# Kernel optimization log

Measured on AMD Instinct MI355X. Metric: run time of the kernel, lower is better.

The kernel has to match this reference:

```python
import jax, jax.numpy as jnp
import numpy as np
import math

B, S, H, NH = 2, 2048, 2048, 16
HD = H // NH            # head_dim = 128
SEQ_LENGTH = 1024       # config.seq_length (logn base)
NEG = -1e9


def _rotate_half(x):
    # x: [..., hd]; split into two halves (j=2 layout) and rotate
    d = x.shape[-1] // 2
    x1, x2 = x[..., :d], x[..., d:]
    return jnp.concatenate([-x2, x1], axis=-1)


def _apply_rope(t, cos, sin):
    # t: [B,S,NH,HD], cos/sin: [1,S,1,rot_dim]; rot_dim == HD here (no pass-through)
    return t * cos + _rotate_half(t) * sin


def setup_inputs() -> dict:
    key = jax.random.key(0)
    k0, k1, k2 = jax.random.split(key, 3)
    hidden_states = jax.random.normal(k0, (B, S, H), jnp.float32)

    # rotary cos/sin: QWen-style, freqs duplicated across both halves
    pos = jnp.arange(S, dtype=jnp.float32)
    inv_freq = 1.0 / (10000.0 ** (jnp.arange(0, HD, 2, dtype=jnp.float32) / HD))  # [HD/2]
    ang = pos[:, None] * inv_freq[None, :]                # [S, HD/2]
    ang = jnp.concatenate([ang, ang], axis=-1)[None, :, None, :]  # [1,S,1,HD]
    cos, sin = jnp.cos(ang), jnp.sin(ang)

    # additive causal mask (registered_causal_mask path is unused in _attn)
    causal = jnp.tril(jnp.ones((S, S), dtype=bool))
    attention_mask = jnp.where(causal, 0.0, NEG)[None, None, :, :].astype(jnp.float32)

    # logn scaling vector for positions 1..S
    i = np.arange(1, S + 1)
    logn_np = np.where(i > SEQ_LENGTH, np.log(i) / np.log(SEQ_LENGTH), 1.0).astype(np.float32)
    logn = jnp.asarray(logn_np)[None, :, None, None]      # [1,S,1,1]

    Wc = jax.random.normal(k1, (H, 3 * H), jnp.float32) * 0.02
    bc = jnp.zeros((3 * H,), jnp.float32)
    Wp = jax.random.normal(k2, (H, H), jnp.float32) * 0.02
    bp = jnp.zeros((H,), jnp.float32)
    return {
        "hidden_states": hidden_states, "cos": cos, "sin": sin,
        "attention_mask": attention_mask, "logn": logn,
        "Wc": Wc, "bc": bc, "Wp": Wp, "bp": bp,
    }


def reference(hidden_states, cos, sin, attention_mask, logn, Wc, bc, Wp, bp):
    # QKV projection
    qkv = hidden_states @ Wc + bc                         # [B,S,3H]
    q, k, v = jnp.split(qkv, 3, axis=-1)
    q = q.reshape(B, S, NH, HD)
    k = k.reshape(B, S, NH, HD)
    v = v.reshape(B, S, NH, HD)

    # rotary embedding on q and k
    q = _apply_rope(q, cos, sin)
    k = _apply_rope(k, cos, sin)

    # logn attention scaling (eval mode): q *= log_{seq_length}(pos) for pos>seq_length
    q = q * logn

    # [B,NH,S,HD]
    q = q.transpose(0, 2, 1, 3)
    k = k.transpose(0, 2, 1, 3)
    v = v.transpose(0, 2, 1, 3)

    scale = 1.0 / math.sqrt(HD)
    scores = jnp.einsum("bhqd,bhkd->bhqk", q, k) * scale + attention_mask
    attn = jax.nn.softmax(scores, axis=-1)
    ctx = jnp.einsum("bhqk,bhkd->bhqd", attn, v)          # [B,NH,S,HD]
    ctx = ctx.transpose(0, 2, 1, 3).reshape(B, S, H)      # merge heads
    return ctx @ Wp + bp                                  # [B,S,H]
```

## Files before the change

### kernel.cpp

```cpp
#include <hip/hip_runtime.h>

#define Bsz 2
#define Ssz 2048
#define Hsz 2048
#define NHsz 16
#define HDsz 128
#define K3sz 6144
#define Msz 4096

typedef _Float16 f16x8 __attribute__((ext_vector_type(8)));
typedef float f32x4 __attribute__((ext_vector_type(4)));

__global__ __launch_bounds__(256)
void cvt_f32_f16(const float* __restrict__ in, _Float16* __restrict__ out) {
  size_t i = ((size_t)blockIdx.x * 256 + threadIdx.x) * 8;
  float4 a = *(const float4*)(in + i);
  float4 b = *(const float4*)(in + i + 4);
  f16x8 v;
  v[0] = (_Float16)a.x; v[1] = (_Float16)a.y; v[2] = (_Float16)a.z; v[3] = (_Float16)a.w;
  v[4] = (_Float16)b.x; v[5] = (_Float16)b.y; v[6] = (_Float16)b.z; v[7] = (_Float16)b.w;
  *(f16x8*)(out + i) = v;
}

__global__ __launch_bounds__(256)
void wtrans(const float* __restrict__ W, _Float16* __restrict__ WT, int N, int K) {
  __shared__ _Float16 T[64][72];
  const int t = threadIdx.x;
  const int n0 = blockIdx.x * 64, k0 = blockIdx.y * 64;
#pragma unroll
  for (int i = 0; i < 4; ++i) {
    int c = i * 256 + t;
    int rr = c >> 4, c4 = c & 15;
    float4 v = *(const float4*)(W + (size_t)(k0 + rr) * N + n0 + c4 * 4);
    T[c4 * 4 + 0][rr] = (_Float16)v.x;
    T[c4 * 4 + 1][rr] = (_Float16)v.y;
    T[c4 * 4 + 2][rr] = (_Float16)v.z;
    T[c4 * 4 + 3][rr] = (_Float16)v.w;
  }
  __syncthreads();
#pragma unroll
  for (int i = 0; i < 2; ++i) {
    int c = i * 256 + t;
    int nn = c >> 3, k8 = c & 7;
    *(f16x8*)(WT + (size_t)(n0 + nn) * K + k0 + k8 * 8) = *(const f16x8*)&T[nn][k8 * 8];
  }
}

template<typename CT>
__global__ __launch_bounds__(256)
void gemm_f16(const _Float16* __restrict__ A, int lda,
              const _Float16* __restrict__ BT,
              const float* __restrict__ bias,
              CT* __restrict__ C, int ldc, int K) {
  __shared__ _Float16 As[128][72];
  __shared__ _Float16 Bs[128][72];
  const int t = threadIdx.x;
  const int w = t >> 6, l = t & 63, lg = l >> 4, ll = l & 15;
  const int wr = w >> 1, wc = w & 1;
  const int m0 = blockIdx.y * 128, c0 = blockIdx.x * 128;

  f32x4 acc[4][4];
#pragma unroll
  for (int mf = 0; mf < 4; ++mf)
#pragma unroll
    for (int nf = 0; nf < 4; ++nf)
#pragma unroll
      for (int r = 0; r < 4; ++r) acc[mf][nf][r] = 0.f;

  for (int k0 = 0; k0 < K; k0 += 64) {
#pragma unroll
    for (int i = 0; i < 4; ++i) {
      int c = i * 256 + t;
      int row = c >> 3, c8 = c & 7;
      *(f16x8*)&As[row][c8 * 8] = *(const f16x8*)(A  + (size_t)(m0 + row) * lda + k0 + c8 * 8);
      *(f16x8*)&Bs[row][c8 * 8] = *(const f16x8*)(BT + (size_t)(c0 + row) * K   + k0 + c8 * 8);
    }
    __syncthreads();
#pragma unroll
    for (int ks = 0; ks < 2; ++ks) {
      f16x8 af[4], bf[4];
#pragma unroll
      for (int x = 0; x < 4; ++x) {
        af[x] = *(const f16x8*)&As[wr * 64 + x * 16 + ll][ks * 32 + lg * 8];
        bf[x] = *(const f16x8*)&Bs[wc * 64 + x * 16 + ll][ks * 32 + lg * 8];
      }
#pragma unroll
      for (int mf = 0; mf < 4; ++mf)
#pragma unroll
        for (int nf = 0; nf < 4; ++nf)
          acc[mf][nf] = __builtin_amdgcn_mfma_f32_16x16x32_f16(af[mf], bf[nf], acc[mf][nf], 0, 0, 0);
    }
    __syncthreads();
  }
#pragma unroll
  for (int mf = 0; mf < 4; ++mf)
#pragma unroll
    for (int nf = 0; nf < 4; ++nf) {
      int col = c0 + wc * 64 + nf * 16 + ll;
      float bv = bias[col];
#pragma unroll
      for (int r = 0; r < 4; ++r) {
        int row = m0 + wr * 64 + mf * 16 + lg * 4 + r;
        C[(size_t)row * ldc + col] = (CT)(acc[mf][nf][r] + bv);
      }
    }
}

__global__ __launch_bounds__(256)
void rope_cvt(_Float16* __restrict__ qkv, const float* __restrict__ cosb,
              const float* __restrict__ sinb, const float* __restrict__ logn,
              _Float16* __restrict__ Kh) {
  int idx = blockIdx.x * 256 + threadIdx.x;
  int d = idx & 63;
  int h = (idx >> 6) & 15;
  int s = (idx >> 10) & 2047;
  int b = idx >> 21;
  size_t base = ((size_t)(b * Ssz + s)) * K3sz + h * HDsz;
  float c1 = cosb[s * HDsz + d];
  float s1 = sinb[s * HDsz + d];
  float c2 = cosb[s * HDsz + 64 + d];
  float s2 = sinb[s * HDsz + 64 + d];
  float ln = logn[s] * 0.08838834764831845f;
  float q1 = (float)qkv[base + d], q2 = (float)qkv[base + 64 + d];
  float k1 = (float)qkv[base + Hsz + d], k2 = (float)qkv[base + Hsz + 64 + d];
  qkv[base + d]      = (_Float16)((q1 * c1 - q2 * s1) * ln);
  qkv[base + 64 + d] = (_Float16)((q2 * c2 + q1 * s2) * ln);
  size_t ko = ((size_t)((b * NHsz + h) * Ssz + s)) * HDsz;
  Kh[ko + d]      = (_Float16)(k1 * c1 - k2 * s1);
  Kh[ko + 64 + d] = (_Float16)(k2 * c2 + k1 * s2);
}

__global__ __launch_bounds__(256)
void vtrans(const _Float16* __restrict__ qkv, _Float16* __restrict__ Vt) {
  __shared__ _Float16 T[128][72];
  const int t = threadIdx.x;
  const int s0 = blockIdx.x * 64;
  const int h = blockIdx.y;
  const int b = blockIdx.z;
#pragma unroll
  for (int i = 0; i < 4; ++i) {
    int c = i * 256 + t;
    int rr = c >> 4, c8 = c & 15;
    f16x8 v = *(const f16x8*)(qkv + ((size_t)(b * Ssz + s0 + rr)) * K3sz + 2 * Hsz + h * HDsz + c8 * 8);
#pragma unroll
    for (int j = 0; j < 8; ++j) T[c8 * 8 + j][rr] = v[j];
  }
  __syncthreads();
  _Float16* Vg = Vt + (size_t)(b * NHsz + h) * (Ssz * HDsz);
#pragma unroll
  for (int i = 0; i < 4; ++i) {
    int c = i * 256 + t;
    int d = c >> 3, s8 = c & 7;
    *(f16x8*)(Vg + (size_t)d * Ssz + s0 + s8 * 8) = *(const f16x8*)&T[d][s8 * 8];
  }
}

__global__ __launch_bounds__(256)
void flash_mfma(_Float16* __restrict__ qkv, const _Float16* __restrict__ Kh,
                const _Float16* __restrict__ Vt) {
  __shared__ _Float16 Ks[64][136];
  __shared__ _Float16 Vs[128][72];
  __shared__ _Float16 Ps[4][16][72];
  const int t = threadIdx.x;
  const int w = t >> 6;
  const int l = t & 63;
  const int lg = l >> 4;
  const int ll = l & 15;
  const int qblk = 31 - (int)blockIdx.x;
  const int h = blockIdx.y;
  const int b = blockIdx.z;
  const size_t bh = (size_t)(b * NHsz + h);

  const int qrow_g = qblk * 64 + w * 16 + ll;
  f16x8 qf[4];
  {
    const _Float16* qrow = qkv + ((size_t)(b * Ssz) + qrow_g) * K3sz + h * HDsz;
#pragma unroll
    for (int kds = 0; kds < 4; ++kds)
      qf[kds] = *(const f16x8*)(qrow + kds * 32 + lg * 8);
  }

  f32x4 O[8];
#pragma unroll
  for (int nf = 0; nf < 8; ++nf)
#pragma unroll
    for (int r = 0; r < 4; ++r) O[nf][r] = 0.f;
  float m[4] = {-1e30f, -1e30f, -1e30f, -1e30f};
  float lsum[4] = {0.f, 0.f, 0.f, 0.f};

  const _Float16* Kg = Kh + bh * (size_t)(Ssz * HDsz);
  const _Float16* Vg = Vt + bh * (size_t)(Ssz * HDsz);

  for (int kt = 0; kt <= qblk; ++kt) {
#pragma unroll
    for (int i = 0; i < 4; ++i) {
      int c = i * 256 + t;
      int rr = c >> 4, c8 = c & 15;
      *(f16x8*)&Ks[rr][c8 * 8] = *(const f16x8*)(Kg + (size_t)(kt * 64 + rr) * HDsz + c8 * 8);
    }
#pragma unroll
    for (int i = 0; i < 4; ++i) {
      int c = i * 256 + t;
      int d = c >> 3, s8 = c & 7;
      *(f16x8*)&Vs[d][s8 * 8] = *(const f16x8*)(Vg + (size_t)d * Ssz + kt * 64 + s8 * 8);
    }
    __syncthreads();

    f32x4 S[4];
#pragma unroll
    for (int kf = 0; kf < 4; ++kf) {
#pragma unroll
      for (int r = 0; r < 4; ++r) S[kf][r] = 0.f;
#pragma unroll
      for (int kds = 0; kds < 4; ++kds) {
        f16x8 bk = *(const f16x8*)&Ks[kf * 16 + ll][kds * 32 + lg * 8];
        S[kf] = __builtin_amdgcn_mfma_f32_16x16x32_f16(qf[kds], bk, S[kf], 0, 0, 0);
      }
    }
    if (kt == qblk) {
#pragma unroll
      for (int kf = 0; kf < 4; ++kf) {
        int kcol = kt * 64 + kf * 16 + ll;
#pragma unroll
        for (int r = 0; r < 4; ++r) {
          int qg = qblk * 64 + w * 16 + lg * 4 + r;
          if (kcol > qg) S[kf][r] = -1e30f;
        }
      }
    }
#pragma unroll
    for (int r = 0; r < 4; ++r) {
      float v = fmaxf(fmaxf(S[0][r], S[1][r]), fmaxf(S[2][r], S[3][r]));
      v = fmaxf(v, __shfl_xor(v, 1));
      v = fmaxf(v, __shfl_xor(v, 2));
      v = fmaxf(v, __shfl_xor(v, 4));
      v = fmaxf(v, __shfl_xor(v, 8));
      float mn = fmaxf(m[r], v);
      float corr = __expf(m[r] - mn);
      float p0 = __expf(S[0][r] - mn);
      float p1 = __expf(S[1][r] - mn);
      float p2 = __expf(S[2][r] - mn);
      float p3 = __expf(S[3][r] - mn);
      float ps = (p0 + p1) + (p2 + p3);
      ps += __shfl_xor(ps, 1);
      ps += __shfl_xor(ps, 2);
      ps += __shfl_xor(ps, 4);
      ps += __shfl_xor(ps, 8);
      lsum[r] = lsum[r] * corr + ps;
      m[r] = mn;
#pragma unroll
      for (int nf = 0; nf < 8; ++nf) O[nf][r] *= corr;
      Ps[w][lg * 4 + r][0 * 16 + ll] = (_Float16)p0;
      Ps[w][lg * 4 + r][1 * 16 + ll] = (_Float16)p1;
      Ps[w][lg * 4 + r][2 * 16 + ll] = (_Float16)p2;
      Ps[w][lg * 4 + r][3 * 16 + ll] = (_Float16)p3;
    }
    f16x8 pa0 = *(const f16x8*)&Ps[w][ll][lg * 8];
    f16x8 pa1 = *(const f16x8*)&Ps[w][ll][32 + lg * 8];
#pragma unroll
    for (int nf = 0; nf < 8; ++nf) {
      f16x8 vb0 = *(const f16x8*)&Vs[nf * 16 + ll][lg * 8];
      f16x8 vb1 = *(const f16x8*)&Vs[nf * 16 + ll][32 + lg * 8];
      O[nf] = __builtin_amdgcn_mfma_f32_16x16x32_f16(pa0, vb0, O[nf], 0, 0, 0);
      O[nf] = __builtin_amdgcn_mfma_f32_16x16x32_f16(pa1, vb1, O[nf], 0, 0, 0);
    }
    __syncthreads();
  }

#pragma unroll
  for (int r = 0; r < 4; ++r) {
    float inv = 1.f / lsum[r];
    _Float16* crow = qkv + ((size_t)(b * Ssz) + qblk * 64 + w * 16 + lg * 4 + r) * K3sz + h * HDsz;
#pragma unroll
    for (int nf = 0; nf < 8; ++nf)
      crow[nf * 16 + ll] = (_Float16)(O[nf][r] * inv);
  }
}

extern "C" void kernel_launch(void* const* d_in, const int* in_sizes, int n_in,
                              void* d_out, int out_size, void* d_ws, size_t ws_size,
                              hipStream_t stream) {
  const float* hs   = (const float*)d_in[0];
  const float* cosb = (const float*)d_in[1];
  const float* sinb = (const float*)d_in[2];
  const float* logn = (const float*)d_in[4];
  const float* Wc   = (const float*)d_in[5];
  const float* bc   = (const float*)d_in[6];
  const float* Wp   = (const float*)d_in[7];
  const float* bp   = (const float*)d_in[8];
  float* out = (float*)d_out;

  _Float16* qkv  = (_Float16*)d_ws;
  _Float16* hsF  = qkv  + (size_t)Msz * K3sz;
  _Float16* WcT  = hsF  + (size_t)Msz * Hsz;
  _Float16* WpT  = WcT  + (size_t)K3sz * Hsz;
  _Float16* Kh   = WpT  + (size_t)Hsz * Hsz;
  _Float16* Vt   = Kh   + (size_t)Bsz * NHsz * Ssz * HDsz;

  cvt_f32_f16<<<(Msz * Hsz) / (256 * 8), 256, 0, stream>>>(hs, hsF);
  { dim3 g(K3sz / 64, Hsz / 64); wtrans<<<g, 256, 0, stream>>>(Wc, WcT, K3sz, Hsz); }
  { dim3 g(Hsz / 64, Hsz / 64);  wtrans<<<g, 256, 0, stream>>>(Wp, WpT, Hsz, Hsz); }

  {
    dim3 g(K3sz / 128, Msz / 128);
    gemm_f16<_Float16><<<g, 256, 0, stream>>>(hsF, Hsz, WcT, bc, qkv, K3sz, Hsz);
  }
  rope_cvt<<<(Bsz * Ssz * NHsz * 64) / 256, 256, 0, stream>>>(qkv, cosb, sinb, logn, Kh);
  {
    dim3 g(Ssz / 64, NHsz, Bsz);
    vtrans<<<g, 256, 0, stream>>>(qkv, Vt);
  }
  {
    dim3 g(Ssz / 64, NHsz, Bsz);
    flash_mfma<<<g, 256, 0, stream>>>(qkv, Kh, Vt);
  }
  {
    dim3 g(Hsz / 128, Msz / 128);
    gemm_f16<float><<<g, 256, 0, stream>>>(qkv, K3sz, WpT, bp, out, Hsz, Hsz);
  }
}
```

Before: 533.4 us.

## Use async global-to-LDS loads with XOR swizzle and lazy softmax rescaling

Replaces the register-staged global-to-shared copies in the GEMM and flash attention kernels with direct global_load_lds 16-byte async copies. Padding is dropped and an XOR swizzle is applied to avoid LDS bank conflicts. Flash attention also skips the running-max rescale unless some row's max grows by more than 8, and defers the row-sum shuffle reduction to the end. This cuts VGPR traffic, LDS footprint and per-tile exp/shuffle work, at the cost of more complex indexing and some risk of fp16 overflow in P from the stale max.

```diff
diff --git a/kernel.cpp b/kernel.cpp
--- a/kernel.cpp
+++ b/kernel.cpp
@@ -10,6 +10,12 @@
 
 typedef _Float16 f16x8 __attribute__((ext_vector_type(8)));
 typedef float f32x4 __attribute__((ext_vector_type(4)));
+
+typedef __attribute__((address_space(3))) void lds_void;
+typedef __attribute__((address_space(1))) void glob_void;
+__device__ __forceinline__ void async_copy16(void* lds, const void* g) {
+  __builtin_amdgcn_global_load_lds((const glob_void*)g, (lds_void*)lds, 16, 0, 0);
+}
 
 __global__ __launch_bounds__(256)
 void cvt_f32_f16(const float* __restrict__ in, _Float16* __restrict__ out) {
@@ -52,13 +58,18 @@
               const _Float16* __restrict__ BT,
               const float* __restrict__ bias,
               CT* __restrict__ C, int ldc, int K) {
-  __shared__ _Float16 As[128][72];
-  __shared__ _Float16 Bs[128][72];
+  __shared__ _Float16 As[128][64];
+  __shared__ _Float16 Bs[128][64];
   const int t = threadIdx.x;
   const int w = t >> 6, l = t & 63, lg = l >> 4, ll = l & 15;
   const int wr = w >> 1, wc = w & 1;
   const int m0 = blockIdx.y * 128, c0 = blockIdx.x * 128;
 
+  const int srow = l >> 3;
+  const int swz = ((l & 7) ^ (srow & 7)) * 8;
+  const size_t aRow = (size_t)(m0 + w * 32 + srow);
+  const size_t bRow = (size_t)(c0 + w * 32 + srow);
+
   f32x4 acc[4][4];
 #pragma unroll
   for (int mf = 0; mf < 4; ++mf)
@@ -70,10 +81,9 @@
   for (int k0 = 0; k0 < K; k0 += 64) {
 #pragma unroll
     for (int i = 0; i < 4; ++i) {
-      int c = i * 256 + t;
-      int row = c >> 3, c8 = c & 7;
-      *(f16x8*)&As[row][c8 * 8] = *(const f16x8*)(A  + (size_t)(m0 + row) * lda + k0 + c8 * 8);
-      *(f16x8*)&Bs[row][c8 * 8] = *(const f16x8*)(BT + (size_t)(c0 + row) * K   + k0 + c8 * 8);
+      int ldsOff = (w * 32 + i * 8) * 128 + l * 16;
+      async_copy16((char*)As + ldsOff, A  + (aRow + i * 8) * lda + k0 + swz);
+      async_copy16((char*)Bs + ldsOff, BT + (bRow + i * 8) * K   + k0 + swz);
     }
     __syncthreads();
 #pragma unroll
@@ -81,8 +91,9 @@
       f16x8 af[4], bf[4];
 #pragma unroll
       for (int x = 0; x < 4; ++x) {
-        af[x] = *(const f16x8*)&As[wr * 64 + x * 16 + ll][ks * 32 + lg * 8];
-        bf[x] = *(const f16x8*)&Bs[wc * 64 + x * 16 + ll][ks * 32 + lg * 8];
+        int cA = ((ks * 4 + lg) ^ (ll & 7)) * 8;
+        af[x] = *(const f16x8*)&As[wr * 64 + x * 16 + ll][cA];
+        bf[x] = *(const f16x8*)&Bs[wc * 64 + x * 16 + ll][cA];
       }
 #pragma unroll
       for (int mf = 0; mf < 4; ++mf)
@@ -158,17 +169,13 @@
 __global__ __launch_bounds__(256)
 void flash_mfma(_Float16* __restrict__ qkv, const _Float16* __restrict__ Kh,
                 const _Float16* __restrict__ Vt) {
-  __shared__ _Float16 Ks[64][136];
-  __shared__ _Float16 Vs[128][72];
-  __shared__ _Float16 Ps[4][16][72];
+  __shared__ _Float16 Ks[64][128];
+  __shared__ _Float16 Vs[128][64];
+  __shared__ _Float16 Ps[4][16][64];
   const int t = threadIdx.x;
-  const int w = t >> 6;
-  const int l = t & 63;
-  const int lg = l >> 4;
-  const int ll = l & 15;
+  const int w = t >> 6, l = t & 63, lg = l >> 4, ll = l & 15;
   const int qblk = 31 - (int)blockIdx.x;
-  const int h = blockIdx.y;
-  const int b = blockIdx.z;
+  const int h = blockIdx.y, b = blockIdx.z;
   const size_t bh = (size_t)(b * NHsz + h);
 
   const int qrow_g = qblk * 64 + w * 16 + ll;
@@ -186,23 +193,29 @@
 #pragma unroll
     for (int r = 0; r < 4; ++r) O[nf][r] = 0.f;
   float m[4] = {-1e30f, -1e30f, -1e30f, -1e30f};
-  float lsum[4] = {0.f, 0.f, 0.f, 0.f};
+  float lp[4] = {0.f, 0.f, 0.f, 0.f};
 
   const _Float16* Kg = Kh + bh * (size_t)(Ssz * HDsz);
   const _Float16* Vg = Vt + bh * (size_t)(Ssz * HDsz);
 
+  int kSrc[4], kLds[4], vSrc[4], vLds[4];
+#pragma unroll
+  for (int i = 0; i < 4; ++i) {
+    int krow = w * 16 + i * 4 + (l >> 4);
+    kSrc[i] = krow * 128 + (((l & 15) ^ (krow & 7)) * 8);
+    kLds[i] = (w * 16 + i * 4) * 256 + l * 16;
+    int vrow = w * 32 + i * 8 + (l >> 3);
+    vSrc[i] = vrow * Ssz + (((l & 7) ^ (vrow & 7)) * 8);
+    vLds[i] = (w * 32 + i * 8) * 128 + l * 16;
+  }
+
   for (int kt = 0; kt <= qblk; ++kt) {
+    const _Float16* Ktile = Kg + (size_t)kt * (64 * HDsz);
+    const _Float16* Vtile = Vg + kt * 64;
 #pragma unroll
     for (int i = 0; i < 4; ++i) {
-      int c = i * 256 + t;
-      int rr = c >> 4, c8 = c & 15;
-      *(f16x8*)&Ks[rr][c8 * 8] = *(const f16x8*)(Kg + (size_t)(kt * 64 + rr) * HDsz + c8 * 8);
-    }
-#pragma unroll
-    for (int i = 0; i < 4; ++i) {
-      int c = i * 256 + t;
-      int d = c >> 3, s8 = c & 7;
-      *(f16x8*)&Vs[d][s8 * 8] = *(const f16x8*)(Vg + (size_t)d * Ssz + kt * 64 + s8 * 8);
+      async_copy16((char*)Ks + kLds[i], Ktile + kSrc[i]);
+      async_copy16((char*)Vs + vLds[i], Vtile + vSrc[i]);
     }
     __syncthreads();
 
@@ -213,7 +226,7 @@
       for (int r = 0; r < 4; ++r) S[kf][r] = 0.f;
 #pragma unroll
       for (int kds = 0; kds < 4; ++kds) {
-        f16x8 bk = *(const f16x8*)&Ks[kf * 16 + ll][kds * 32 + lg * 8];
+        f16x8 bk = *(const f16x8*)&Ks[kf * 16 + ll][(((kds * 4 + lg) ^ (ll & 7))) * 8];
         S[kf] = __builtin_amdgcn_mfma_f32_16x16x32_f16(qf[kds], bk, S[kf], 0, 0, 0);
       }
     }
@@ -228,6 +241,9 @@
         }
       }
     }
+
+    float pmax[4];
+    bool need = false;
 #pragma unroll
     for (int r = 0; r < 4; ++r) {
       float v = fmaxf(fmaxf(S[0][r], S[1][r]), fmaxf(S[2][r], S[3][r]));
@@ -235,32 +251,40 @@
       v = fmaxf(v, __shfl_xor(v, 2));
       v = fmaxf(v, __shfl_xor(v, 4));
       v = fmaxf(v, __shfl_xor(v, 8));
-      float mn = fmaxf(m[r], v);
-      float corr = __expf(m[r] - mn);
-      float p0 = __expf(S[0][r] - mn);
-      float p1 = __expf(S[1][r] - mn);
-      float p2 = __expf(S[2][r] - mn);
-      float p3 = __expf(S[3][r] - mn);
-      float ps = (p0 + p1) + (p2 + p3);
-      ps += __shfl_xor(ps, 1);
-      ps += __shfl_xor(ps, 2);
-      ps += __shfl_xor(ps, 4);
-      ps += __shfl_xor(ps, 8);
-      lsum[r] = lsum[r] * corr + ps;
-      m[r] = mn;
-#pragma unroll
-      for (int nf = 0; nf < 8; ++nf) O[nf][r] *= corr;
-      Ps[w][lg * 4 + r][0 * 16 + ll] = (_Float16)p0;
-      Ps[w][lg * 4 + r][1 * 16 + ll] = (_Float16)p1;
-      Ps[w][lg * 4 + r][2 * 16 + ll] = (_Float16)p2;
-      Ps[w][lg * 4 + r][3 * 16 + ll] = (_Float16)p3;
-    }
-    f16x8 pa0 = *(const f16x8*)&Ps[w][ll][lg * 8];
-    f16x8 pa1 = *(const f16x8*)&Ps[w][ll][32 + lg * 8];
+      pmax[r] = v;
+      need = need || (v > m[r] + 8.f);
+    }
+    if (__any(need)) {
+#pragma unroll
+      for (int r = 0; r < 4; ++r) {
+        float mn = fmaxf(m[r], pmax[r]);
+        float corr = __expf(m[r] - mn);
+        lp[r] *= corr;
+#pragma unroll
+        for (int nf = 0; nf < 8; ++nf) O[nf][r] *= corr;
+        m[r] = mn;
+      }
+    }
+#pragma unroll
+    for (int r = 0; r < 4; ++r) {
+      int q7 = (lg * 4 + r) & 7;
+      float p0 = __expf(S[0][r] - m[r]);
+      float p1 = __expf(S[1][r] - m[r]);
+      float p2 = __expf(S[2][r] - m[r]);
+      float p3 = __expf(S[3][r] - m[r]);
+      lp[r] += (p0 + p1) + (p2 + p3);
+      int u = ll >> 3, s = ll & 7;
+      Ps[w][lg * 4 + r][((0 + u) ^ q7) * 8 + s] = (_Float16)p0;
+      Ps[w][lg * 4 + r][((2 + u) ^ q7) * 8 + s] = (_Float16)p1;
+      Ps[w][lg * 4 + r][((4 + u) ^ q7) * 8 + s] = (_Float16)p2;
+      Ps[w][lg * 4 + r][((6 + u) ^ q7) * 8 + s] = (_Float16)p3;
+    }
+    f16x8 pa0 = *(const f16x8*)&Ps[w][ll][((lg ^ (ll & 7))) * 8];
+    f16x8 pa1 = *(const f16x8*)&Ps[w][ll][(((4 + lg) ^ (ll & 7))) * 8];
 #pragma unroll
     for (int nf = 0; nf < 8; ++nf) {
-      f16x8 vb0 = *(const f16x8*)&Vs[nf * 16 + ll][lg * 8];
-      f16x8 vb1 = *(const f16x8*)&Vs[nf * 16 + ll][32 + lg * 8];
+      f16x8 vb0 = *(const f16x8*)&Vs[nf * 16 + ll][((lg ^ (ll & 7))) * 8];
+      f16x8 vb1 = *(const f16x8*)&Vs[nf * 16 + ll][(((4 + lg) ^ (ll & 7))) * 8];
       O[nf] = __builtin_amdgcn_mfma_f32_16x16x32_f16(pa0, vb0, O[nf], 0, 0, 0);
       O[nf] = __builtin_amdgcn_mfma_f32_16x16x32_f16(pa1, vb1, O[nf], 0, 0, 0);
     }
@@ -269,7 +293,12 @@
 
 #pragma unroll
   for (int r = 0; r < 4; ++r) {
-    float inv = 1.f / lsum[r];
+    float s = lp[r];
+    s += __shfl_xor(s, 1);
+    s += __shfl_xor(s, 2);
+    s += __shfl_xor(s, 4);
+    s += __shfl_xor(s, 8);
+    float inv = 1.f / s;
     _Float16* crow = qkv + ((size_t)(b * Ssz) + qblk * 64 + w * 16 + lg * 4 + r) * K3sz + h * HDsz;
 #pragma unroll
     for (int nf = 0; nf < 8; ++nf)
```

After: 495.8 us. -7.1%, faster.
